# Kernel optimization log

Hardware: AMD Instinct MI355X
Metric: run time of the kernel (lower is better)

The kernel has to match this reference:

```python
import jax, jax.numpy as jnp
import numpy as np

ALPHA = 0.2  # LeakyReLU negative slope
NEG_INF = -9e15


def setup_inputs() -> dict:
    key = jax.random.key(0)
    k1, k2, k3, k4 = jax.random.split(key, 4)
    B, N, F_IN, F_OUT = 2, 4096, 128, 64
    h = jax.random.normal(k1, (B, N, F_IN), dtype=jnp.float32)
    adj = jax.random.randint(k2, (N, N), 0, 2, dtype=jnp.int32)
    W = jax.random.normal(k3, (F_IN, F_OUT), dtype=jnp.float32) * (1.414 / np.sqrt(F_IN))
    a = jax.random.normal(k4, (2 * F_OUT, 1), dtype=jnp.float32) * 0.1
    return {"h": h, "adj": adj, "W": W, "a": a}


def reference(h, adj, W, a):
    # h: (B, N, F_in), adj: (N, N), W: (F_in, F_out), a: (2*F_out, 1)
    Wh = jnp.einsum("bnf,fo->bno", h, W)  # (B, N, F_out)
    F_out = W.shape[1]
    a1 = a[:F_out, 0]   # attends to source node i
    a2 = a[F_out:, 0]   # attends to target node j
    # e_ij = leakyrelu(a1.Wh_i + a2.Wh_j)  -- rank-1 decomposition of the
    # original cat([Wh_i, Wh_j]) @ a, identical math without O(N^2*2F) tensor.
    s1 = Wh @ a1  # (B, N)
    s2 = Wh @ a2  # (B, N)
    e = s1[:, :, None] + s2[:, None, :]  # (B, N, N)
    e = jnp.where(e >= 0, e, ALPHA * e)  # LeakyReLU
    scores = jnp.where(adj[None, :, :] > 0, e, NEG_INF)
    attention = jax.nn.softmax(scores, axis=-1)
    # dropout=0 (eval/deterministic baseline)
    h_prime = jnp.einsum("bij,bjo->bio", attention, Wh)  # (B, N, F_out)
    return jax.nn.elu(h_prime)  # concat=True branch
```

## Files before the change

### kernel.cpp

```cpp
#include <hip/hip_runtime.h>
#include <hip/hip_bf16.h>
#include <math.h>

#define NB 2
#define NN 4096
#define FIN 128
#define FOUT 64
#define LALPHA 0.2f

#define WS_S1    0
#define WS_S2    (NB*NN)
#define WS_WHT   (2*NB*NN)
#define WS_ABITS (WS_WHT + NB*FOUT*NN/2)


typedef __attribute__((ext_vector_type(8))) short short8;
typedef __attribute__((ext_vector_type(4))) float f32x4;

static __device__ inline unsigned int pack2bf(float x, float y) {
    float2 f2; f2.x = x; f2.y = y;
    __hip_bfloat162 pp = __float22bfloat162_rn(f2);
    return *reinterpret_cast<unsigned int*>(&pp);
}

#define GLL16(gsrc, ldst)                                                        \
    __builtin_amdgcn_global_load_lds(                                            \
        (const __attribute__((address_space(1))) void*)(gsrc),                   \
        (__attribute__((address_space(3))) void*)(ldst), 16, 0, 0)

__global__ __launch_bounds__(256) void k1_proj(const float* __restrict__ h,
                                               const float* __restrict__ W,
                                               const float* __restrict__ a,
                                               const int* __restrict__ adj,
                                               float* __restrict__ ws) {
    __shared__ __align__(16) float hbuf[4][128];
    __shared__ float tbuf[4][68];
    int gid  = blockIdx.x * 256 + threadIdx.x;
    int wid  = gid >> 6;
    int lane = threadIdx.x & 63;
    int w    = threadIdx.x >> 6;

    int prow = 2 * blockIdx.x + (w >> 1);
    const int4* psrc = (const int4*)(adj + (size_t)prow * NN + (w & 1) * 2048);
    int4 pv[8];
#pragma unroll
    for (int k = 0; k < 8; ++k) pv[k] = psrc[k * 64 + lane];

    const float* hrow = h + (size_t)wid * FIN;
    hbuf[w][lane]      = hrow[lane];
    hbuf[w][64 + lane] = hrow[64 + lane];

    float acc = 0.f;
#pragma unroll
    for (int f4 = 0; f4 < 32; ++f4) {
        float4 hv = *(const float4*)&hbuf[w][f4 * 4];
        acc = fmaf(hv.x, W[(f4 * 4 + 0) * FOUT + lane], acc);
        acc = fmaf(hv.y, W[(f4 * 4 + 1) * FOUT + lane], acc);
        acc = fmaf(hv.z, W[(f4 * 4 + 2) * FOUT + lane], acc);
        acc = fmaf(hv.w, W[(f4 * 4 + 3) * FOUT + lane], acc);
    }
    tbuf[w][lane] = acc;
    float v1 = acc * a[lane];
    float v2 = acc * a[FOUT + lane];
#pragma unroll
    for (int off = 32; off; off >>= 1) {
        v1 += __shfl_xor(v1, off);
        v2 += __shfl_xor(v2, off);
    }
    if (lane == 0) {
        ws[WS_S1 + wid] = v1 * 1.44269504088896f;
        ws[WS_S2 + wid] = v2 * 1.44269504088896f;
    }

    unsigned int* ab = (unsigned int*)(ws + WS_ABITS);
#pragma unroll
    for (int k = 0; k < 8; ++k) {
        unsigned int nib = (pv[k].x != 0 ? 1u : 0u)
                         | (pv[k].y != 0 ? 2u : 0u)
                         | (pv[k].z != 0 ? 4u : 0u)
                         | (pv[k].w != 0 ? 8u : 0u);
        unsigned int val = nib << ((lane & 7) * 4);
        val |= __shfl_xor(val, 1);
        val |= __shfl_xor(val, 2);
        val |= __shfl_xor(val, 4);
        if ((lane & 7) == 0)
            ab[(size_t)prow * 128 + (w & 1) * 64 + k * 8 + (lane >> 3)] = val;
    }

    __syncthreads();
    if (threadIdx.x < 64) {
        int f = threadIdx.x;
        int wid0 = blockIdx.x * 4;
        int b  = wid0 >> 12;
        int n0 = wid0 & (NN - 1);
        unsigned short* whT = (unsigned short*)(ws + WS_WHT);
        uint2 pk;
        pk.x = pack2bf(tbuf[0][f], tbuf[1][f]);
        pk.y = pack2bf(tbuf[2][f], tbuf[3][f]);
        size_t off = ((size_t)(b * 128 + (n0 >> 5)) * 2048) + f * 32 + (n0 & 31);
        *(uint2*)&whT[off] = pk;
    }
}

__global__ __launch_bounds__(1024, 4) void k3_attn(const float* __restrict__ ws,
                                                   float* __restrict__ out) {
    __shared__ float redbuf[16 * 2048];
    __shared__ float s2buf[16][256];
    __shared__ float lred[16][32];
    const int tid  = threadIdx.x;
    const int w    = tid >> 6;
    const int lane = tid & 63;
    const int col  = lane & 15;
    const int quad = lane >> 4;
    const int rt   = blockIdx.x >> 1;
    const int b    = blockIdx.x & 1;
    const int i0   = rt * 32;
    const int jbase = w * 256;

    const float* __restrict__ s1 = ws + WS_S1 + b * NN;
    const float* __restrict__ s2 = ws + WS_S2 + b * NN;
    const unsigned short* __restrict__ whT =
        (const unsigned short*)(ws + WS_WHT) + (size_t)b * FOUT * NN;
    const unsigned int* __restrict__ abits = (const unsigned int*)(ws + WS_ABITS);

    char* slot = (char*)redbuf + w * 8192;
    float* s2s = s2buf[w];
    const unsigned short* wsrc = whT + (size_t)w * 8 * 2048;
    const int lsrc = col * 32 + quad * 8;

    unsigned int mrow[2][8];
#pragma unroll
    for (int g = 0; g < 2; ++g) {
        const int4* mp = (const int4*)&abits[(size_t)(i0 + g * 16 + col) * 128 + w * 8];
        *(int4*)&mrow[g][0] = mp[0];
        *(int4*)&mrow[g][4] = mp[1];
    }
    float s1a[2];
#pragma unroll
    for (int g = 0; g < 2; ++g) s1a[g] = s1[i0 + g * 16 + col];
    asm volatile("s_waitcnt vmcnt(0)" ::: "memory");

#define ISSUE_TILE(ks, sl)                                                \
    do {                                                                  \
        const unsigned short* wb_ = wsrc + (size_t)(ks) * 2048;           \
        GLL16(wb_ + 0 * 512 + lsrc, slot + (sl) * 4096 + 0 * 1024);       \
        GLL16(wb_ + 1 * 512 + lsrc, slot + (sl) * 4096 + 1 * 1024);       \
        GLL16(wb_ + 2 * 512 + lsrc, slot + (sl) * 4096 + 2 * 1024);       \
        GLL16(wb_ + 3 * 512 + lsrc, slot + (sl) * 4096 + 3 * 1024);       \
    } while (0)

    GLL16(&s2[jbase] + lane * 4, s2s);
    ISSUE_TILE(0, 0);
    ISSUE_TILE(1, 1);
    asm volatile("s_waitcnt vmcnt(8)" ::: "memory");

    f32x4 acc[2][4];
    float lsum[2] = {0.f, 0.f};
#pragma unroll
    for (int g = 0; g < 2; ++g)
#pragma unroll
        for (int nt = 0; nt < 4; ++nt) acc[g][nt] = (f32x4)0.f;

#pragma unroll
    for (int ks = 0; ks < 8; ++ks) {
        const int sl = ks & 1;

        float4 s2lo = *(const float4*)&s2s[ks * 32 + quad * 8];
        float4 s2hi = *(const float4*)&s2s[ks * 32 + quad * 8 + 4];
        float sj[8] = {s2lo.x, s2lo.y, s2lo.z, s2lo.w,
                       s2hi.x, s2hi.y, s2hi.z, s2hi.w};
        short8 afrag[2];
#pragma unroll
        for (int g = 0; g < 2; ++g) {
            const unsigned int mb = (mrow[g][ks] >> (quad * 8)) & 0xffu;
            float p[8];
#pragma unroll
            for (int jj = 0; jj < 8; ++jj) {
                float e = s1a[g] + sj[jj];
                e = fmaxf(e, LALPHA * e);
                float pe = exp2f(e);
                p[jj] = ((mb >> jj) & 1u) ? pe : 0.f;
                lsum[g] += p[jj];
            }
            unsigned int pk[4];
#pragma unroll
            for (int q = 0; q < 4; ++q) pk[q] = pack2bf(p[2 * q], p[2 * q + 1]);
            afrag[g] = *(short8*)pk;
        }

        __builtin_amdgcn_sched_barrier(0);
        if (ks == 7) asm volatile("s_waitcnt vmcnt(0)" ::: "memory");
        else         asm volatile("s_waitcnt vmcnt(4)" ::: "memory");

        __builtin_amdgcn_s_setprio(1);
#pragma unroll
        for (int nt = 0; nt < 4; ++nt) {
            short8 bf = *(const short8*)(slot + sl * 4096 + nt * 1024 + lane * 16);
            acc[0][nt] = __builtin_amdgcn_mfma_f32_16x16x32_bf16(
                afrag[0], bf, acc[0][nt], 0, 0, 0);
            acc[1][nt] = __builtin_amdgcn_mfma_f32_16x16x32_bf16(
                afrag[1], bf, acc[1][nt], 0, 0, 0);
        }
        __builtin_amdgcn_s_setprio(0);
        if (ks < 6) ISSUE_TILE(ks + 2, sl);
    }

    float* red_w = redbuf + w * 2048;
#pragma unroll
    for (int g = 0; g < 2; ++g) {
        float v = lsum[g];
        v += __shfl_xor(v, 16);
        v += __shfl_xor(v, 32);
        if (quad == 0) lred[w][g * 16 + col] = v;
#pragma unroll
        for (int nt = 0; nt < 4; ++nt)
#pragma unroll
            for (int reg = 0; reg < 4; ++reg)
                red_w[g * 1024 + ((nt * 4 + reg) << 6) + lane] = acc[g][nt][reg];
    }
    __syncthreads();

#pragma unroll
    for (int e = 0; e < 2; ++e) {
        int flat = e * 1024 + tid;
        int f    = flat & 63;
        int r32  = flat >> 6;
        int g    = r32 >> 4;
        int r16  = r32 & 15;
        int q2   = r16 >> 2, reg = r16 & 3;
        int c2   = f & 15,   nt  = f >> 4;
        int ln   = q2 * 16 + c2;
        int off  = g * 1024 + ((nt * 4 + reg) << 6) + ln;
        float acv = 0.f, l = 0.f;
#pragma unroll
        for (int ww = 0; ww < 16; ++ww) {
            acv += redbuf[ww * 2048 + off];
            l   += lred[ww][g * 16 + r16];
        }
        float v = acv / l;
        out[((size_t)(b * NN + i0 + r32) << 6) + f] = v > 0.f ? v : (__expf(v) - 1.f);
    }
}

extern "C" void kernel_launch(void* const* d_in, const int* in_sizes, int n_in,
                              void* d_out, int out_size, void* d_ws, size_t ws_size,
                              hipStream_t stream) {
    const float* h   = (const float*)d_in[0];
    const int*   adj = (const int*)d_in[1];
    const float* W   = (const float*)d_in[2];
    const float* a   = (const float*)d_in[3];
    float* ws  = (float*)d_ws;
    float* out = (float*)d_out;

    hipLaunchKernelGGL(k1_proj, dim3(NB * NN / 4), dim3(256), 0, stream, h, W, a, adj, ws);
    hipLaunchKernelGGL(k3_attn, dim3(256), dim3(1024), 0, stream, ws, out);
}
```

Measured before the change: 135.7 us.

## Retile attention to 64-row blocks with split-J and a separate finalize kernel

Each attention block now processes 64 rows over half of the key range (split-J across two blocks) instead of 32 rows over the full range. Each B tile loaded from LDS now feeds four MFMAs instead of two, which halves the Wh tile traffic per row. Partial numerators and denominators are reduced across waves with a tree in LDS, written to a workspace slab, and combined by a new small k4_fin kernel that applies normalization and ELU. exp2f is also replaced by the raw v_exp_f32 instruction. The cost is an extra kernel launch, extra global round trips for the partial results, more accumulator registers, and several more block-wide syncs in the tree reduction.

```diff
diff --git a/kernel.cpp b/kernel.cpp
--- a/kernel.cpp
+++ b/kernel.cpp
@@ -12,6 +12,7 @@
 #define WS_S2    (NB*NN)
 #define WS_WHT   (2*NB*NN)
 #define WS_ABITS (WS_WHT + NB*FOUT*NN/2)
+#define WS_SLAB  (WS_ABITS + NN*128)
 
 
 typedef __attribute__((ext_vector_type(8))) short short8;
@@ -21,6 +22,12 @@
     float2 f2; f2.x = x; f2.y = y;
     __hip_bfloat162 pp = __float22bfloat162_rn(f2);
     return *reinterpret_cast<unsigned int*>(&pp);
+}
+
+static __device__ inline float fast_exp2(float x) {
+    float r;
+    asm("v_exp_f32 %0, %1" : "=v"(r) : "v"(x));
+    return r;
 }
 
 #define GLL16(gsrc, ldst)                                                        \
@@ -102,20 +109,21 @@
     }
 }
 
-__global__ __launch_bounds__(1024, 4) void k3_attn(const float* __restrict__ ws,
-                                                   float* __restrict__ out) {
+__global__ __launch_bounds__(1024, 4) void k3_attn(float* __restrict__ ws) {
     __shared__ float redbuf[16 * 2048];
     __shared__ float s2buf[16][256];
-    __shared__ float lred[16][32];
+    __shared__ float lred[16][64];
     const int tid  = threadIdx.x;
     const int w    = tid >> 6;
     const int lane = tid & 63;
     const int col  = lane & 15;
     const int quad = lane >> 4;
-    const int rt   = blockIdx.x >> 1;
-    const int b    = blockIdx.x & 1;
-    const int i0   = rt * 32;
-    const int jbase = w * 256;
+    const int jc   = blockIdx.x & 1;
+    const int t6   = blockIdx.x >> 1;
+    const int b    = t6 >> 6;
+    const int i0   = (t6 & 63) * 64;
+    const int jbase = jc * 2048 + w * 128;
+    const int tile0 = jc * 64 + w * 4;
 
     const float* __restrict__ s1 = ws + WS_S1 + b * NN;
     const float* __restrict__ s2 = ws + WS_S2 + b * NN;
@@ -123,21 +131,19 @@
         (const unsigned short*)(ws + WS_WHT) + (size_t)b * FOUT * NN;
     const unsigned int* __restrict__ abits = (const unsigned int*)(ws + WS_ABITS);
 
-    char* slot = (char*)redbuf + w * 8192;
+    char* slot = (char*)(redbuf + w * 2048);
     float* s2s = s2buf[w];
-    const unsigned short* wsrc = whT + (size_t)w * 8 * 2048;
+    const unsigned short* wsrc = whT + (size_t)tile0 * 2048;
     const int lsrc = col * 32 + quad * 8;
 
-    unsigned int mrow[2][8];
-#pragma unroll
-    for (int g = 0; g < 2; ++g) {
-        const int4* mp = (const int4*)&abits[(size_t)(i0 + g * 16 + col) * 128 + w * 8];
-        *(int4*)&mrow[g][0] = mp[0];
-        *(int4*)&mrow[g][4] = mp[1];
-    }
-    float s1a[2];
-#pragma unroll
-    for (int g = 0; g < 2; ++g) s1a[g] = s1[i0 + g * 16 + col];
+    unsigned int mrow[4][4];
+#pragma unroll
+    for (int g = 0; g < 4; ++g)
+        *(int4*)&mrow[g][0] =
+            *(const int4*)&abits[(size_t)(i0 + g * 16 + col) * 128 + tile0];
+    float s1a[4];
+#pragma unroll
+    for (int g = 0; g < 4; ++g) s1a[g] = s1[i0 + g * 16 + col];
     asm volatile("s_waitcnt vmcnt(0)" ::: "memory");
 
 #define ISSUE_TILE(ks, sl)                                                \
@@ -154,31 +160,31 @@
     ISSUE_TILE(1, 1);
     asm volatile("s_waitcnt vmcnt(8)" ::: "memory");
 
-    f32x4 acc[2][4];
-    float lsum[2] = {0.f, 0.f};
-#pragma unroll
-    for (int g = 0; g < 2; ++g)
+    f32x4 acc[4][4];
+    float lsum[4] = {0.f, 0.f, 0.f, 0.f};
+#pragma unroll
+    for (int g = 0; g < 4; ++g)
 #pragma unroll
         for (int nt = 0; nt < 4; ++nt) acc[g][nt] = (f32x4)0.f;
 
 #pragma unroll
-    for (int ks = 0; ks < 8; ++ks) {
+    for (int ks = 0; ks < 4; ++ks) {
         const int sl = ks & 1;
 
         float4 s2lo = *(const float4*)&s2s[ks * 32 + quad * 8];
         float4 s2hi = *(const float4*)&s2s[ks * 32 + quad * 8 + 4];
         float sj[8] = {s2lo.x, s2lo.y, s2lo.z, s2lo.w,
                        s2hi.x, s2hi.y, s2hi.z, s2hi.w};
-        short8 afrag[2];
-#pragma unroll
-        for (int g = 0; g < 2; ++g) {
+        short8 afrag[4];
+#pragma unroll
+        for (int g = 0; g < 4; ++g) {
             const unsigned int mb = (mrow[g][ks] >> (quad * 8)) & 0xffu;
             float p[8];
 #pragma unroll
             for (int jj = 0; jj < 8; ++jj) {
                 float e = s1a[g] + sj[jj];
                 e = fmaxf(e, LALPHA * e);
-                float pe = exp2f(e);
+                float pe = fast_exp2(e);
                 p[jj] = ((mb >> jj) & 1u) ? pe : 0.f;
                 lsum[g] += p[jj];
             }
@@ -189,57 +195,87 @@
         }
 
         __builtin_amdgcn_sched_barrier(0);
-        if (ks == 7) asm volatile("s_waitcnt vmcnt(0)" ::: "memory");
+        if (ks == 3) asm volatile("s_waitcnt vmcnt(0)" ::: "memory");
         else         asm volatile("s_waitcnt vmcnt(4)" ::: "memory");
 
         __builtin_amdgcn_s_setprio(1);
 #pragma unroll
         for (int nt = 0; nt < 4; ++nt) {
             short8 bf = *(const short8*)(slot + sl * 4096 + nt * 1024 + lane * 16);
-            acc[0][nt] = __builtin_amdgcn_mfma_f32_16x16x32_bf16(
-                afrag[0], bf, acc[0][nt], 0, 0, 0);
-            acc[1][nt] = __builtin_amdgcn_mfma_f32_16x16x32_bf16(
-                afrag[1], bf, acc[1][nt], 0, 0, 0);
+            acc[0][nt] = __builtin_amdgcn_mfma_f32_16x16x32_bf16(afrag[0], bf, acc[0][nt], 0, 0, 0);
+            acc[1][nt] = __builtin_amdgcn_mfma_f32_16x16x32_bf16(afrag[1], bf, acc[1][nt], 0, 0, 0);
+            acc[2][nt] = __builtin_amdgcn_mfma_f32_16x16x32_bf16(afrag[2], bf, acc[2][nt], 0, 0, 0);
+            acc[3][nt] = __builtin_amdgcn_mfma_f32_16x16x32_bf16(afrag[3], bf, acc[3][nt], 0, 0, 0);
         }
         __builtin_amdgcn_s_setprio(0);
-        if (ks < 6) ISSUE_TILE(ks + 2, sl);
-    }
-
-    float* red_w = redbuf + w * 2048;
-#pragma unroll
-    for (int g = 0; g < 2; ++g) {
+        if (ks < 2) ISSUE_TILE(ks + 2, sl);
+    }
+
+#pragma unroll
+    for (int g = 0; g < 4; ++g) {
         float v = lsum[g];
         v += __shfl_xor(v, 16);
         v += __shfl_xor(v, 32);
         if (quad == 0) lred[w][g * 16 + col] = v;
-#pragma unroll
-        for (int nt = 0; nt < 4; ++nt)
-#pragma unroll
-            for (int reg = 0; reg < 4; ++reg)
-                red_w[g * 1024 + ((nt * 4 + reg) << 6) + lane] = acc[g][nt][reg];
-    }
-    __syncthreads();
-
-#pragma unroll
-    for (int e = 0; e < 2; ++e) {
-        int flat = e * 1024 + tid;
-        int f    = flat & 63;
-        int r32  = flat >> 6;
-        int g    = r32 >> 4;
-        int r16  = r32 & 15;
-        int q2   = r16 >> 2, reg = r16 & 3;
-        int c2   = f & 15,   nt  = f >> 4;
-        int ln   = q2 * 16 + c2;
-        int off  = g * 1024 + ((nt * 4 + reg) << 6) + ln;
-        float acv = 0.f, l = 0.f;
-#pragma unroll
-        for (int ww = 0; ww < 16; ++ww) {
-            acv += redbuf[ww * 2048 + off];
-            l   += lred[ww][g * 16 + r16];
-        }
-        float v = acv / l;
-        out[((size_t)(b * NN + i0 + r32) << 6) + f] = v > 0.f ? v : (__expf(v) - 1.f);
-    }
+    }
+
+#pragma unroll
+    for (int half = 8; half >= 1; half >>= 1) {
+        __syncthreads();
+        if (w >= half && w < 2 * half) {
+#pragma unroll
+            for (int g = 0; g < 4; ++g)
+#pragma unroll
+                for (int nt = 0; nt < 4; ++nt)
+#pragma unroll
+                    for (int reg = 0; reg < 4; ++reg)
+                        redbuf[(w - half) * 4096 + ((g * 4 + nt) * 4 + reg) * 64 + lane]
+                            = acc[g][nt][reg];
+        }
+        __syncthreads();
+        if (w < half) {
+#pragma unroll
+            for (int g = 0; g < 4; ++g)
+#pragma unroll
+                for (int nt = 0; nt < 4; ++nt)
+#pragma unroll
+                    for (int reg = 0; reg < 4; ++reg)
+                        acc[g][nt][reg]
+                            += redbuf[w * 4096 + ((g * 4 + nt) * 4 + reg) * 64 + lane];
+        }
+    }
+
+    if (w == 0) {
+        float* sb = ws + WS_SLAB + (size_t)blockIdx.x * 4160;
+#pragma unroll
+        for (int g = 0; g < 4; ++g)
+#pragma unroll
+            for (int nt = 0; nt < 4; ++nt)
+                *(f32x4*)&sb[(((g * 4 + nt) * 64) + lane) * 4] = acc[g][nt];
+        float lt = 0.f;
+#pragma unroll
+        for (int ww = 0; ww < 16; ++ww) lt += lred[ww][lane];
+        sb[4096 + lane] = lt;
+    }
+}
+
+__global__ __launch_bounds__(256) void k4_fin(const float* __restrict__ ws,
+                                              float* __restrict__ out) {
+    int n    = blockIdx.x * 256 + threadIdx.x;
+    int f    = n & 63;
+    int grow = n >> 6;
+    int t6   = grow >> 6;
+    int r64  = grow & 63;
+    int g    = r64 >> 4, quad = (r64 >> 2) & 3, reg = r64 & 3;
+    int nt   = f >> 4,  col  = f & 15;
+    int lane = quad * 16 + col;
+    const float* s0 = ws + WS_SLAB + (size_t)(t6 * 2 + 0) * 4160;
+    const float* s1 = ws + WS_SLAB + (size_t)(t6 * 2 + 1) * 4160;
+    int idx = (((g * 4 + nt) * 64) + lane) * 4 + reg;
+    float acv = s0[idx] + s1[idx];
+    float l   = s0[4096 + r64] + s1[4096 + r64];
+    float v = acv / l;
+    out[n] = v > 0.f ? v : (__expf(v) - 1.f);
 }
 
 extern "C" void kernel_launch(void* const* d_in, const int* in_sizes, int n_in,
@@ -253,5 +289,6 @@
     float* out = (float*)d_out;
 
     hipLaunchKernelGGL(k1_proj, dim3(NB * NN / 4), dim3(256), 0, stream, h, W, a, adj, ws);
-    hipLaunchKernelGGL(k3_attn, dim3(256), dim3(1024), 0, stream, ws, out);
-}
+    hipLaunchKernelGGL(k3_attn, dim3(256), dim3(1024), 0, stream, ws);
+    hipLaunchKernelGGL(k4_fin,  dim3(NB * NN * FOUT / 256), dim3(256), 0, stream, ws, out);
+}
```

Result: slower. 168.3 us (+24.0%).
